# Optimization experiments

Measured on AMD Instinct MI355X. Metric: run time of the kernel, lower is better.

Reference implementation:

```python
import jax, jax.numpy as jnp
import numpy as np

B, P, D = 4, 1024, 1024
H, DQK, DV = 16, 64, 64
DMID = 4096
EPS = 1e-5


def _layernorm(x, g, b):
    mu = jnp.mean(x, axis=-1, keepdims=True)
    var = jnp.mean(jnp.square(x - mu), axis=-1, keepdims=True)
    return (x - mu) * jax.lax.rsqrt(var + EPS) * g + b


def setup_inputs() -> dict:
    key = jax.random.key(0)
    ks = jax.random.split(key, 12)
    s = 0.02
    return {
        "x": jax.random.normal(ks[0], (B, P, D), jnp.float32),
        "attn_prev": jax.random.normal(ks[1], (B, H, P, P), jnp.float32),
        "Wq": jax.random.normal(ks[2], (H * DQK, D), jnp.float32) * s,
        "Wk": jax.random.normal(ks[3], (H * DQK, D), jnp.float32) * s,
        "Wv": jax.random.normal(ks[4], (H * DV, D), jnp.float32) * s,
        "W_th": jax.random.normal(ks[5], (H, H), jnp.float32) * (1.0 / H) + jnp.eye(H, dtype=jnp.float32),
        "Wpv": jax.random.normal(ks[6], (D, H * DV), jnp.float32) * s,
        "W1": jax.random.normal(ks[7], (DMID, D), jnp.float32) * s,
        "b1": jnp.zeros((DMID,), jnp.float32),
        "W2": jax.random.normal(ks[8], (D, DMID // 2), jnp.float32) * s,
        "b2": jnp.zeros((D,), jnp.float32),
        "ln1_g": jnp.ones((D,), jnp.float32),
        "ln1_b": jnp.zeros((D,), jnp.float32),
        "ln2_g": jnp.ones((D,), jnp.float32),
        "ln2_b": jnp.zeros((D,), jnp.float32),
    }


def reference(x, attn_prev, Wq, Wk, Wv, W_th, Wpv, W1, b1, W2, b2, ln1_g, ln1_b, ln2_g, ln2_b):
    b, p, d = x.shape
    scale = jnp.sqrt(jnp.asarray(DQK, x.dtype))
    # projections, reshaped to (B, P, H, dh)
    q = (x @ Wq.T).reshape(b, p, H, DQK) / scale
    k = (x @ Wk.T).reshape(b, p, H, DQK)
    v = (x @ Wv.T).reshape(b, p, H, DV)
    # raw scores (B, H, P, P)
    scores = jnp.einsum("bqhd,bkhd->bhqk", q, k)
    # talking-heads: 1x1 conv over head channels == head mixing matrix
    scores = jnp.einsum("gh,bhqk->bgqk", W_th, scores)
    # realformer residual on scores, then softmax
    attn = jax.nn.softmax(scores + attn_prev, axis=-1)
    o = jnp.einsum("bhqk,bkhd->bqhd", attn, v).reshape(b, p, H * DV)
    x_sa = o @ Wpv.T
    x1 = _layernorm(x + x_sa, ln1_g, ln1_b)
    # GLU FFN
    h = x1 @ W1.T + b1
    a, g = h[..., : DMID // 2], h[..., DMID // 2 :]
    y = (a * jax.nn.relu(g)) @ W2.T + b2
    out = _layernorm(x1 + y, ln2_g, ln2_b)
    return (out, attn)
```

## Files before the change

### kernel.cpp

```cpp
#include <hip/hip_runtime.h>

typedef __attribute__((ext_vector_type(4))) float f32x4;
typedef __attribute__((ext_vector_type(8))) __bf16 bf16x8;
typedef __attribute__((ext_vector_type(8))) unsigned short u16x8;

__device__ __forceinline__ unsigned short f2bf(float f) {
    union { float f; unsigned int u; } v; v.f = f;
    unsigned int r = v.u + 0x7FFFu + ((v.u >> 16) & 1u);
    return (unsigned short)(r >> 16);
}
__device__ __forceinline__ float bf2f(unsigned short u) {
    union { unsigned int u; float f; } v; v.u = ((unsigned int)u) << 16; return v.f;
}

__device__ __forceinline__ void async16(const void* g, void* l) {
    __builtin_amdgcn_global_load_lds((const __attribute__((address_space(1))) void*)g,
                                     (__attribute__((address_space(3))) void*)l, 16, 0, 0);
}

__global__ __launch_bounds__(256) void cast_bf16_kernel(const float* __restrict__ in,
                                                        unsigned short* __restrict__ out,
                                                        int n4, float scale) {
    int i = blockIdx.x * 256 + threadIdx.x;
    if (i >= n4) return;
    float4 f = ((const float4*)in)[i];
    ushort4 u;
    u.x = f2bf(f.x * scale); u.y = f2bf(f.y * scale);
    u.z = f2bf(f.z * scale); u.w = f2bf(f.w * scale);
    ((ushort4*)out)[i] = u;
}

template <int OUTMODE, int BIAS, int RESMODE>
__global__ __launch_bounds__(256) void gemm_bt(const unsigned short* __restrict__ A,
                                               const unsigned short* __restrict__ B,
                                               void* __restrict__ C,
                                               const float* __restrict__ bias,
                                               const void* __restrict__ res,
                                               int K, int lda, int ldb, int ldc,
                                               int Hc, long sAh, long sAb, long sBh, long sBb,
                                               long sCh, long sCb) {
    __shared__ unsigned short As[128 * 32];
    __shared__ unsigned short Bs[128 * 32];
    const int t = threadIdx.x;
    const int m0 = blockIdx.y * 128, n0 = blockIdx.x * 128;
    const long z = blockIdx.z;
    const long zh = z % Hc, zb = z / Hc;
    const unsigned short* Ab = A + zh * sAh + zb * sAb + (long)m0 * lda;
    const unsigned short* Bb = B + zh * sBh + zb * sBb + (long)n0 * ldb;
    const long cbase = zh * sCh + zb * sCb;

    const int l = t & 63, w = t >> 6;
    const int lane16 = l & 15, quad = l >> 4;
    const int wm = w >> 1, wn = w & 1;
    const int aoff = (wm * 64 + lane16) * 32 + quad * 8;
    const int boff = (wn * 64 + lane16) * 32 + quad * 8;

    f32x4 acc[4][4];
#pragma unroll
    for (int i = 0; i < 4; ++i)
#pragma unroll
        for (int j = 0; j < 4; ++j) acc[i][j] = (f32x4){0.f, 0.f, 0.f, 0.f};

    for (int k0 = 0; k0 < K; k0 += 32) {
#pragma unroll
        for (int i = 0; i < 2; ++i) {
            int c = i * 256 + t;
            async16(Ab + (long)(c >> 2) * lda + k0 + (c & 3) * 8, &As[c * 8]);
        }
#pragma unroll
        for (int i = 0; i < 2; ++i) {
            int c = i * 256 + t;
            async16(Bb + (long)(c >> 2) * ldb + k0 + (c & 3) * 8, &Bs[c * 8]);
        }
        __syncthreads();
        bf16x8 af[4], bv[4];
#pragma unroll
        for (int mt = 0; mt < 4; ++mt) af[mt] = *(const bf16x8*)&As[aoff + mt * 512];
#pragma unroll
        for (int nt = 0; nt < 4; ++nt) bv[nt] = *(const bf16x8*)&Bs[boff + nt * 512];
#pragma unroll
        for (int mt = 0; mt < 4; ++mt)
#pragma unroll
            for (int nt = 0; nt < 4; ++nt)
                acc[mt][nt] = __builtin_amdgcn_mfma_f32_16x16x32_bf16(af[mt], bv[nt], acc[mt][nt], 0, 0, 0);
        __syncthreads();
    }

#pragma unroll
    for (int mt = 0; mt < 4; ++mt) {
#pragma unroll
        for (int nt = 0; nt < 4; ++nt) {
            int col = n0 + wn * 64 + nt * 16 + lane16;
            int row0 = m0 + wm * 64 + mt * 16 + quad * 4;
#pragma unroll
            for (int r = 0; r < 4; ++r) {
                long ri = (long)(row0 + r) * ldc + col;
                float v = acc[mt][nt][r];
                if (BIAS) v += bias[col];
                if (RESMODE == 1) v += ((const float*)res)[ri];
                if (RESMODE == 2) v += bf2f(((const unsigned short*)res)[ri]);
                if (OUTMODE == 1) ((unsigned short*)C)[cbase + ri] = f2bf(v);
                else              ((float*)C)[cbase + ri] = v;
            }
        }
    }
}

__global__ __launch_bounds__(256) void transpose_v(const unsigned short* __restrict__ qkvb,
                                                   unsigned short* __restrict__ vT) {
    __shared__ unsigned short tile[64 * 72];
    const int t = threadIdx.x;
    const int k0 = blockIdx.x * 64;
    const int z = blockIdx.y;
    const int b = z >> 4, h = z & 15;
    const unsigned short* src = qkvb + ((long)b * 1024 + k0) * 3072 + 2048 + h * 64;
#pragma unroll
    for (int i = 0; i < 2; ++i) {
        int idx = i * 256 + t, k = idx >> 3, c = idx & 7;
        u16x8 v = *(const u16x8*)(src + (long)k * 3072 + c * 8);
        *(u16x8*)&tile[k * 72 + c * 8] = v;
    }
    __syncthreads();
    unsigned short* dst = vT + (long)z * 65536 + k0;
#pragma unroll
    for (int i = 0; i < 2; ++i) {
        int idx = i * 256 + t, d = idx >> 3, c = idx & 7;
        u16x8 o8;
#pragma unroll
        for (int j = 0; j < 8; ++j) o8[j] = tile[(c * 8 + j) * 72 + d];
        *(u16x8*)&dst[(long)d * 1024 + c * 8] = o8;
    }
}

__global__ __launch_bounds__(256) void mix_softmax(float* __restrict__ attn,
                                                   const float* __restrict__ prev,
                                                   const float* __restrict__ Wth) {
    __shared__ float sW[256];
    __shared__ float red[4][16];
    const int t = threadIdx.x;
    const int q = blockIdx.x, b = blockIdx.y;
    sW[t] = Wth[t];
    __syncthreads();
    const long base = (long)b * 16777216 + (long)q * 1024;

    float val[4][16];
    float gmax[16];
#pragma unroll
    for (int g = 0; g < 16; ++g) gmax[g] = -1e30f;

#pragma unroll
    for (int kk = 0; kk < 4; ++kk) {
        int k = kk * 256 + t;
        float s[16];
#pragma unroll
        for (int h = 0; h < 16; ++h) s[h] = attn[base + (long)h * 1048576 + k];
#pragma unroll
        for (int g = 0; g < 16; ++g) {
            float m = prev[base + (long)g * 1048576 + k];
#pragma unroll
            for (int h = 0; h < 16; ++h) m = fmaf(sW[g * 16 + h], s[h], m);
            val[kk][g] = m;
            gmax[g] = fmaxf(gmax[g], m);
        }
    }
    const int w = t >> 6, l = t & 63;
#pragma unroll
    for (int g = 0; g < 16; ++g) {
#pragma unroll
        for (int o = 32; o >= 1; o >>= 1) gmax[g] = fmaxf(gmax[g], __shfl_xor(gmax[g], o));
    }
    if (l == 0) {
#pragma unroll
        for (int g = 0; g < 16; ++g) red[w][g] = gmax[g];
    }
    __syncthreads();
#pragma unroll
    for (int g = 0; g < 16; ++g)
        gmax[g] = fmaxf(fmaxf(red[0][g], red[1][g]), fmaxf(red[2][g], red[3][g]));
    __syncthreads();

    float gsum[16];
#pragma unroll
    for (int g = 0; g < 16; ++g) gsum[g] = 0.f;
#pragma unroll
    for (int kk = 0; kk < 4; ++kk)
#pragma unroll
        for (int g = 0; g < 16; ++g) {
            float e = __expf(val[kk][g] - gmax[g]);
            val[kk][g] = e;
            gsum[g] += e;
        }
#pragma unroll
    for (int g = 0; g < 16; ++g) {
#pragma unroll
        for (int o = 32; o >= 1; o >>= 1) gsum[g] += __shfl_xor(gsum[g], o);
    }
    if (l == 0) {
#pragma unroll
        for (int g = 0; g < 16; ++g) red[w][g] = gsum[g];
    }
    __syncthreads();
#pragma unroll
    for (int g = 0; g < 16; ++g)
        gsum[g] = 1.f / (red[0][g] + red[1][g] + red[2][g] + red[3][g]);
#pragma unroll
    for (int kk = 0; kk < 4; ++kk)
#pragma unroll
        for (int g = 0; g < 16; ++g)
            attn[base + (long)g * 1048576 + kk * 256 + t] = val[kk][g] * gsum[g];
}

__global__ __launch_bounds__(256) void pv_gemm(const float* __restrict__ attn,
                                               const unsigned short* __restrict__ vT,
                                               unsigned short* __restrict__ ob) {
    __shared__ unsigned short As[128 * 32];
    __shared__ unsigned short Bs[64 * 32];
    const int t = threadIdx.x;
    const int m0 = blockIdx.x * 128;
    const int z = blockIdx.y;
    const int b = z >> 4, h = z & 15;
    const float* Ab = attn + (long)z * 1048576 + (long)m0 * 1024;
    const unsigned short* Bb = vT + (long)z * 65536;
    const int l = t & 63, w = t >> 6, lane16 = l & 15, quad = l >> 4;

    f32x4 acc[2][4];
#pragma unroll
    for (int i = 0; i < 2; ++i)
#pragma unroll
        for (int j = 0; j < 4; ++j) acc[i][j] = (f32x4){0.f, 0.f, 0.f, 0.f};

    for (int k0 = 0; k0 < 1024; k0 += 32) {
#pragma unroll
        for (int i = 0; i < 4; ++i) {
            int idx = i * 256 + t, row = idx >> 3, c4 = idx & 7;
            float4 f = *(const float4*)(Ab + (long)row * 1024 + k0 + c4 * 4);
            ushort4 u;
            u.x = f2bf(f.x); u.y = f2bf(f.y); u.z = f2bf(f.z); u.w = f2bf(f.w);
            *(ushort4*)&As[row * 32 + c4 * 4] = u;
        }
        {
            int c = t;
            async16(Bb + (long)(c >> 2) * 1024 + k0 + (c & 3) * 8, &Bs[c * 8]);
        }
        __syncthreads();
        bf16x8 af[2], bv[4];
#pragma unroll
        for (int mt = 0; mt < 2; ++mt)
            af[mt] = *(const bf16x8*)&As[(w * 32 + mt * 16 + lane16) * 32 + quad * 8];
#pragma unroll
        for (int nt = 0; nt < 4; ++nt)
            bv[nt] = *(const bf16x8*)&Bs[(nt * 16 + lane16) * 32 + quad * 8];
#pragma unroll
        for (int mt = 0; mt < 2; ++mt)
#pragma unroll
            for (int nt = 0; nt < 4; ++nt)
                acc[mt][nt] = __builtin_amdgcn_mfma_f32_16x16x32_bf16(af[mt], bv[nt], acc[mt][nt], 0, 0, 0);
        __syncthreads();
    }
#pragma unroll
    for (int mt = 0; mt < 2; ++mt)
#pragma unroll
        for (int nt = 0; nt < 4; ++nt)
#pragma unroll
            for (int r = 0; r < 4; ++r) {
                int gq = m0 + w * 32 + mt * 16 + quad * 4 + r;
                ob[((long)b * 1024 + gq) * 1024 + h * 64 + nt * 16 + lane16] = f2bf(acc[mt][nt][r]);
            }
}

__global__ __launch_bounds__(256) void ln_kernel(const float* __restrict__ in,
                                                 const float* __restrict__ gamma,
                                                 const float* __restrict__ beta,
                                                 unsigned short* __restrict__ outb,
                                                 float* __restrict__ outf) {
    __shared__ float rs[4][2];
    const int row = blockIdx.x, t = threadIdx.x;
    const float* r = in + (long)row * 1024;
    float v[4], s = 0.f, s2 = 0.f;
#pragma unroll
    for (int i = 0; i < 4; ++i) { v[i] = r[i * 256 + t]; s += v[i]; s2 += v[i] * v[i]; }
#pragma unroll
    for (int o = 32; o >= 1; o >>= 1) { s += __shfl_xor(s, o); s2 += __shfl_xor(s2, o); }
    const int w = t >> 6, l = t & 63;
    if (l == 0) { rs[w][0] = s; rs[w][1] = s2; }
    __syncthreads();
    s = rs[0][0] + rs[1][0] + rs[2][0] + rs[3][0];
    s2 = rs[0][1] + rs[1][1] + rs[2][1] + rs[3][1];
    float mu = s * (1.f / 1024.f);
    float var = s2 * (1.f / 1024.f) - mu * mu;
    float rstd = rsqrtf(var + 1e-5f);
#pragma unroll
    for (int i = 0; i < 4; ++i) {
        int col = i * 256 + t;
        float y = (v[i] - mu) * rstd * gamma[col] + beta[col];
        if (outb) outb[(long)row * 1024 + col] = f2bf(y);
        if (outf) outf[(long)row * 1024 + col] = y;
    }
}

__global__ __launch_bounds__(256) void glu_kernel(const unsigned short* __restrict__ h,
                                                  unsigned short* __restrict__ out) {
    int i = blockIdx.x * 256 + threadIdx.x;
    int row = i >> 8, c = i & 255;
    u16x8 a8 = *(const u16x8*)(h + (long)row * 4096 + c * 8);
    u16x8 g8 = *(const u16x8*)(h + (long)row * 4096 + 2048 + c * 8);
    u16x8 o8;
#pragma unroll
    for (int j = 0; j < 8; ++j) {
        float g = bf2f(g8[j]);
        g = g > 0.f ? g : 0.f;
        o8[j] = f2bf(bf2f(a8[j]) * g);
    }
    *(u16x8*)(out + (long)row * 2048 + c * 8) = o8;
}

extern "C" void kernel_launch(void* const* d_in, const int* in_sizes, int n_in,
                              void* d_out, int out_size, void* d_ws, size_t ws_size,
                              hipStream_t stream) {
    const float* x    = (const float*)d_in[0];
    const float* prev = (const float*)d_in[1];
    const float* Wq   = (const float*)d_in[2];
    const float* Wk   = (const float*)d_in[3];
    const float* Wv   = (const float*)d_in[4];
    const float* Wth  = (const float*)d_in[5];
    const float* Wpv  = (const float*)d_in[6];
    const float* W1   = (const float*)d_in[7];
    const float* b1   = (const float*)d_in[8];
    const float* W2   = (const float*)d_in[9];
    const float* b2   = (const float*)d_in[10];
    const float* ln1g = (const float*)d_in[11];
    const float* ln1b = (const float*)d_in[12];
    const float* ln2g = (const float*)d_in[13];
    const float* ln2b = (const float*)d_in[14];

    float* out  = (float*)d_out;
    float* attn = out + 4194304;

    char* ws = (char*)d_ws;
    unsigned short* xb    = (unsigned short*)(ws + 0);
    unsigned short* wqkvb = (unsigned short*)(ws + 8388608);
    unsigned short* wpvb  = (unsigned short*)(ws + 14680064);
    unsigned short* w1b   = (unsigned short*)(ws + 16777216);
    unsigned short* w2b   = (unsigned short*)(ws + 25165824);
    unsigned short* qkvb  = (unsigned short*)(ws + 29360128);
    unsigned short* vTb   = (unsigned short*)(ws + 54525952);
    unsigned short* obuf  = (unsigned short*)(ws + 62914560);
    unsigned short* x1b   = (unsigned short*)(ws + 71303168);
    unsigned short* glub  = (unsigned short*)(ws + 79691776);
    unsigned short* hb    = (unsigned short*)(ws + 96468992);
    float*          pre   = (float*)(ws + 130023424);

    dim3 T(256);
    cast_bf16_kernel<<<4096, T, 0, stream>>>(x, xb, 1048576, 1.f);
    cast_bf16_kernel<<<1024, T, 0, stream>>>(Wq, wqkvb,           262144, 0.125f);
    cast_bf16_kernel<<<1024, T, 0, stream>>>(Wk, wqkvb + 1048576, 262144, 1.f);
    cast_bf16_kernel<<<1024, T, 0, stream>>>(Wv, wqkvb + 2097152, 262144, 1.f);
    cast_bf16_kernel<<<1024, T, 0, stream>>>(Wpv, wpvb,  262144, 1.f);
    cast_bf16_kernel<<<4096, T, 0, stream>>>(W1, w1b,  1048576, 1.f);
    cast_bf16_kernel<<<2048, T, 0, stream>>>(W2, w2b,   524288, 1.f);

    gemm_bt<1, 0, 0><<<dim3(24, 32, 1), T, 0, stream>>>(xb, wqkvb, qkvb, nullptr, nullptr,
        1024, 1024, 1024, 3072, 1, 0, 0, 0, 0, 0, 0);

    transpose_v<<<dim3(16, 64), T, 0, stream>>>(qkvb, vTb);

    gemm_bt<0, 0, 0><<<dim3(8, 8, 64), T, 0, stream>>>(qkvb, qkvb + 1024, attn, nullptr, nullptr,
        64, 3072, 3072, 1024, 16, 64, 3145728, 64, 3145728, 1048576, 16777216);

    mix_softmax<<<dim3(1024, 4), T, 0, stream>>>(attn, prev, Wth);

    pv_gemm<<<dim3(8, 64), T, 0, stream>>>(attn, vTb, obuf);

    gemm_bt<0, 0, 1><<<dim3(8, 32, 1), T, 0, stream>>>(obuf, wpvb, pre, nullptr, x,
        1024, 1024, 1024, 1024, 1, 0, 0, 0, 0, 0, 0);

    ln_kernel<<<4096, T, 0, stream>>>(pre, ln1g, ln1b, x1b, nullptr);

    gemm_bt<1, 1, 0><<<dim3(32, 32, 1), T, 0, stream>>>(x1b, w1b, hb, b1, nullptr,
        1024, 1024, 1024, 4096, 1, 0, 0, 0, 0, 0, 0);

    glu_kernel<<<4096, T, 0, stream>>>(hb, glub);

    gemm_bt<0, 1, 2><<<dim3(8, 32, 1), T, 0, stream>>>(glub, w2b, pre, b2, x1b,
        2048, 2048, 2048, 1024, 1, 0, 0, 0, 0, 0, 0);

    ln_kernel<<<4096, T, 0, stream>>>(pre, ln2g, ln2b, nullptr, out);
}
```

Baseline: 956.9 us.

## Emit bf16 attention in softmax, async-load it in PV GEMM, batch casts

The mix_softmax kernel now processes four contiguous keys per thread with float4 loads and stores, and writes a bf16 copy of the attention probabilities alongside the fp32 output. pv_gemm reads that bf16 copy through async global-to-LDS loads instead of re-reading fp32 attention and converting it in registers. The seven weight and input casts are folded into two multi-segment launches to cut launch overhead. Workspace is repacked so buffers alias, with vT and obuf placed in the not-yet-written output region, which adds an extra bf16 attention write and depends on the ordering of the aliased buffers being correct.

```diff
diff --git a/kernel.cpp b/kernel.cpp
--- a/kernel.cpp
+++ b/kernel.cpp
@@ -18,16 +18,18 @@
                                      (__attribute__((address_space(3))) void*)l, 16, 0, 0);
 }
 
-__global__ __launch_bounds__(256) void cast_bf16_kernel(const float* __restrict__ in,
-                                                        unsigned short* __restrict__ out,
-                                                        int n4, float scale) {
+struct CastSeg { const float* src; unsigned short* dst; int n4; float scale; };
+struct Cast4Args { CastSeg seg[4]; };
+
+__global__ __launch_bounds__(256) void cast_multi(Cast4Args a) {
+    CastSeg s = a.seg[blockIdx.y];
     int i = blockIdx.x * 256 + threadIdx.x;
-    if (i >= n4) return;
-    float4 f = ((const float4*)in)[i];
+    if (i >= s.n4) return;
+    float4 f = ((const float4*)s.src)[i];
     ushort4 u;
-    u.x = f2bf(f.x * scale); u.y = f2bf(f.y * scale);
-    u.z = f2bf(f.z * scale); u.w = f2bf(f.w * scale);
-    ((ushort4*)out)[i] = u;
+    u.x = f2bf(f.x * s.scale); u.y = f2bf(f.y * s.scale);
+    u.z = f2bf(f.z * s.scale); u.w = f2bf(f.w * s.scale);
+    ((ushort4*)s.dst)[i] = u;
 }
 
 template <int OUTMODE, int BIAS, int RESMODE>
@@ -133,6 +135,7 @@
 }
 
 __global__ __launch_bounds__(256) void mix_softmax(float* __restrict__ attn,
+                                                   unsigned short* __restrict__ ab,
                                                    const float* __restrict__ prev,
                                                    const float* __restrict__ Wth) {
     __shared__ float sW[256];
@@ -141,76 +144,73 @@
     const int q = blockIdx.x, b = blockIdx.y;
     sW[t] = Wth[t];
     __syncthreads();
-    const long base = (long)b * 16777216 + (long)q * 1024;
-
-    float val[4][16];
-    float gmax[16];
-#pragma unroll
-    for (int g = 0; g < 16; ++g) gmax[g] = -1e30f;
-
-#pragma unroll
-    for (int kk = 0; kk < 4; ++kk) {
-        int k = kk * 256 + t;
-        float s[16];
-#pragma unroll
-        for (int h = 0; h < 16; ++h) s[h] = attn[base + (long)h * 1048576 + k];
+    const long base = (long)b * 16777216 + (long)q * 1024 + t * 4;
+
+    float4 val[16];
+#pragma unroll
+    for (int g = 0; g < 16; ++g) val[g] = *(const float4*)(prev + base + (long)g * 1048576);
+#pragma unroll
+    for (int h = 0; h < 16; ++h) {
+        float4 s4 = *(const float4*)(attn + base + (long)h * 1048576);
 #pragma unroll
         for (int g = 0; g < 16; ++g) {
-            float m = prev[base + (long)g * 1048576 + k];
-#pragma unroll
-            for (int h = 0; h < 16; ++h) m = fmaf(sW[g * 16 + h], s[h], m);
-            val[kk][g] = m;
-            gmax[g] = fmaxf(gmax[g], m);
+            float wg = sW[g * 16 + h];
+            val[g].x = fmaf(wg, s4.x, val[g].x);
+            val[g].y = fmaf(wg, s4.y, val[g].y);
+            val[g].z = fmaf(wg, s4.z, val[g].z);
+            val[g].w = fmaf(wg, s4.w, val[g].w);
         }
     }
     const int w = t >> 6, l = t & 63;
+    float gm[16];
 #pragma unroll
     for (int g = 0; g < 16; ++g) {
-#pragma unroll
-        for (int o = 32; o >= 1; o >>= 1) gmax[g] = fmaxf(gmax[g], __shfl_xor(gmax[g], o));
+        float m = fmaxf(fmaxf(val[g].x, val[g].y), fmaxf(val[g].z, val[g].w));
+#pragma unroll
+        for (int o = 32; o >= 1; o >>= 1) m = fmaxf(m, __shfl_xor(m, o));
+        gm[g] = m;
     }
     if (l == 0) {
 #pragma unroll
-        for (int g = 0; g < 16; ++g) red[w][g] = gmax[g];
+        for (int g = 0; g < 16; ++g) red[w][g] = gm[g];
     }
     __syncthreads();
 #pragma unroll
     for (int g = 0; g < 16; ++g)
-        gmax[g] = fmaxf(fmaxf(red[0][g], red[1][g]), fmaxf(red[2][g], red[3][g]));
-    __syncthreads();
-
-    float gsum[16];
-#pragma unroll
-    for (int g = 0; g < 16; ++g) gsum[g] = 0.f;
-#pragma unroll
-    for (int kk = 0; kk < 4; ++kk)
-#pragma unroll
-        for (int g = 0; g < 16; ++g) {
-            float e = __expf(val[kk][g] - gmax[g]);
-            val[kk][g] = e;
-            gsum[g] += e;
-        }
+        gm[g] = fmaxf(fmaxf(red[0][g], red[1][g]), fmaxf(red[2][g], red[3][g]));
+    __syncthreads();
+
+    float gs[16];
 #pragma unroll
     for (int g = 0; g < 16; ++g) {
-#pragma unroll
-        for (int o = 32; o >= 1; o >>= 1) gsum[g] += __shfl_xor(gsum[g], o);
+        val[g].x = __expf(val[g].x - gm[g]);
+        val[g].y = __expf(val[g].y - gm[g]);
+        val[g].z = __expf(val[g].z - gm[g]);
+        val[g].w = __expf(val[g].w - gm[g]);
+        float s = (val[g].x + val[g].y) + (val[g].z + val[g].w);
+#pragma unroll
+        for (int o = 32; o >= 1; o >>= 1) s += __shfl_xor(s, o);
+        gs[g] = s;
     }
     if (l == 0) {
 #pragma unroll
-        for (int g = 0; g < 16; ++g) red[w][g] = gsum[g];
-    }
-    __syncthreads();
-#pragma unroll
-    for (int g = 0; g < 16; ++g)
-        gsum[g] = 1.f / (red[0][g] + red[1][g] + red[2][g] + red[3][g]);
-#pragma unroll
-    for (int kk = 0; kk < 4; ++kk)
-#pragma unroll
-        for (int g = 0; g < 16; ++g)
-            attn[base + (long)g * 1048576 + kk * 256 + t] = val[kk][g] * gsum[g];
-}
-
-__global__ __launch_bounds__(256) void pv_gemm(const float* __restrict__ attn,
+        for (int g = 0; g < 16; ++g) red[w][g] = gs[g];
+    }
+    __syncthreads();
+#pragma unroll
+    for (int g = 0; g < 16; ++g) {
+        float inv = 1.f / (red[0][g] + red[1][g] + red[2][g] + red[3][g]);
+        float4 r;
+        r.x = val[g].x * inv; r.y = val[g].y * inv;
+        r.z = val[g].z * inv; r.w = val[g].w * inv;
+        *(float4*)(attn + base + (long)g * 1048576) = r;
+        ushort4 u;
+        u.x = f2bf(r.x); u.y = f2bf(r.y); u.z = f2bf(r.z); u.w = f2bf(r.w);
+        *(ushort4*)(ab + base + (long)g * 1048576) = u;
+    }
+}
+
+__global__ __launch_bounds__(256) void pv_gemm(const unsigned short* __restrict__ ab,
                                                const unsigned short* __restrict__ vT,
                                                unsigned short* __restrict__ ob) {
     __shared__ unsigned short As[128 * 32];
@@ -219,7 +219,7 @@
     const int m0 = blockIdx.x * 128;
     const int z = blockIdx.y;
     const int b = z >> 4, h = z & 15;
-    const float* Ab = attn + (long)z * 1048576 + (long)m0 * 1024;
+    const unsigned short* Ab = ab + (long)z * 1048576 + (long)m0 * 1024;
     const unsigned short* Bb = vT + (long)z * 65536;
     const int l = t & 63, w = t >> 6, lane16 = l & 15, quad = l >> 4;
 
@@ -231,12 +231,9 @@
 
     for (int k0 = 0; k0 < 1024; k0 += 32) {
 #pragma unroll
-        for (int i = 0; i < 4; ++i) {
-            int idx = i * 256 + t, row = idx >> 3, c4 = idx & 7;
-            float4 f = *(const float4*)(Ab + (long)row * 1024 + k0 + c4 * 4);
-            ushort4 u;
-            u.x = f2bf(f.x); u.y = f2bf(f.y); u.z = f2bf(f.z); u.w = f2bf(f.w);
-            *(ushort4*)&As[row * 32 + c4 * 4] = u;
+        for (int i = 0; i < 2; ++i) {
+            int c = i * 256 + t;
+            async16(Ab + (long)(c >> 2) * 1024 + k0 + (c & 3) * 8, &As[c * 8]);
         }
         {
             int c = t;
@@ -336,28 +333,30 @@
     float* out  = (float*)d_out;
     float* attn = out + 4194304;
 
+    unsigned short* vTb  = (unsigned short*)d_out;
+    unsigned short* obuf = (unsigned short*)((char*)d_out + 8388608);
+
     char* ws = (char*)d_ws;
-    unsigned short* xb    = (unsigned short*)(ws + 0);
-    unsigned short* wqkvb = (unsigned short*)(ws + 8388608);
-    unsigned short* wpvb  = (unsigned short*)(ws + 14680064);
-    unsigned short* w1b   = (unsigned short*)(ws + 16777216);
-    unsigned short* w2b   = (unsigned short*)(ws + 25165824);
-    unsigned short* qkvb  = (unsigned short*)(ws + 29360128);
-    unsigned short* vTb   = (unsigned short*)(ws + 54525952);
-    unsigned short* obuf  = (unsigned short*)(ws + 62914560);
-    unsigned short* x1b   = (unsigned short*)(ws + 71303168);
-    unsigned short* glub  = (unsigned short*)(ws + 79691776);
-    unsigned short* hb    = (unsigned short*)(ws + 96468992);
-    float*          pre   = (float*)(ws + 130023424);
+    unsigned short* qkvb  = (unsigned short*)(ws + 0);
+    unsigned short* xb    = (unsigned short*)(ws + 25165824);
+    unsigned short* wqkvb = (unsigned short*)(ws + 33554432);
+    unsigned short* ab    = (unsigned short*)(ws + 0);
+    unsigned short* wpvb  = (unsigned short*)(ws + 0);
+    unsigned short* w1b   = (unsigned short*)(ws + 2097152);
+    unsigned short* w2b   = (unsigned short*)(ws + 10485760);
+    float*          pre   = (float*)(ws + 14680064);
+    unsigned short* x1b   = (unsigned short*)(ws + 31457280);
+    unsigned short* hb    = (unsigned short*)(ws + 39845888);
+    unsigned short* glub  = (unsigned short*)(ws + 73400320);
 
     dim3 T(256);
-    cast_bf16_kernel<<<4096, T, 0, stream>>>(x, xb, 1048576, 1.f);
-    cast_bf16_kernel<<<1024, T, 0, stream>>>(Wq, wqkvb,           262144, 0.125f);
-    cast_bf16_kernel<<<1024, T, 0, stream>>>(Wk, wqkvb + 1048576, 262144, 1.f);
-    cast_bf16_kernel<<<1024, T, 0, stream>>>(Wv, wqkvb + 2097152, 262144, 1.f);
-    cast_bf16_kernel<<<1024, T, 0, stream>>>(Wpv, wpvb,  262144, 1.f);
-    cast_bf16_kernel<<<4096, T, 0, stream>>>(W1, w1b,  1048576, 1.f);
-    cast_bf16_kernel<<<2048, T, 0, stream>>>(W2, w2b,   524288, 1.f);
+
+    Cast4Args c1;
+    c1.seg[0] = { x,  xb,              1048576, 1.f };
+    c1.seg[1] = { Wq, wqkvb,           262144, 0.125f };
+    c1.seg[2] = { Wk, wqkvb + 1048576, 262144, 1.f };
+    c1.seg[3] = { Wv, wqkvb + 2097152, 262144, 1.f };
+    cast_multi<<<dim3(4096, 4), T, 0, stream>>>(c1);
 
     gemm_bt<1, 0, 0><<<dim3(24, 32, 1), T, 0, stream>>>(xb, wqkvb, qkvb, nullptr, nullptr,
         1024, 1024, 1024, 3072, 1, 0, 0, 0, 0, 0, 0);
@@ -367,9 +366,16 @@
     gemm_bt<0, 0, 0><<<dim3(8, 8, 64), T, 0, stream>>>(qkvb, qkvb + 1024, attn, nullptr, nullptr,
         64, 3072, 3072, 1024, 16, 64, 3145728, 64, 3145728, 1048576, 16777216);
 
-    mix_softmax<<<dim3(1024, 4), T, 0, stream>>>(attn, prev, Wth);
-
-    pv_gemm<<<dim3(8, 64), T, 0, stream>>>(attn, vTb, obuf);
+    mix_softmax<<<dim3(1024, 4), T, 0, stream>>>(attn, ab, prev, Wth);
+
+    pv_gemm<<<dim3(8, 64), T, 0, stream>>>(ab, vTb, obuf);
+
+    Cast4Args c2;
+    c2.seg[0] = { Wpv, wpvb, 262144, 1.f };
+    c2.seg[1] = { W1,  w1b, 1048576, 1.f };
+    c2.seg[2] = { W2,  w2b,  524288, 1.f };
+    c2.seg[3] = { Wpv, wpvb, 0, 1.f };
+    cast_multi<<<dim3(4096, 3), T, 0, stream>>>(c2);
 
     gemm_bt<0, 0, 1><<<dim3(8, 32, 1), T, 0, stream>>>(obuf, wpvb, pre, nullptr, x,
         1024, 1024, 1024, 1024, 1, 0, 0, 0, 0, 0, 0);
```

After: 947.6 us. No clear change (-1.0%).
